# Performance work log

Hardware: AMD Instinct MI355X
Metric: run time of the kernel (lower is better)

The kernel has to match this reference:

```python
import jax, jax.numpy as jnp
import numpy as np
import math

B, N, D_IN, D_OUT, H = 8, 1024, 512, 512, 8
DH = D_OUT // H  # 64
SCALE = math.sqrt(DH)

def setup_inputs() -> dict:
    key = jax.random.key(0)
    ks = jax.random.split(key, 10)
    s_in = 1.0 / math.sqrt(D_IN)
    s_out = 1.0 / math.sqrt(D_OUT)
    return {
        "x": jax.random.normal(ks[0], (B, N, D_IN), dtype=jnp.float32),
        "Wq": jax.random.uniform(ks[1], (D_IN, D_OUT), jnp.float32, -s_in, s_in),
        "bq": jnp.zeros((D_OUT,), jnp.float32),
        "Wk": jax.random.uniform(ks[2], (D_IN, D_OUT), jnp.float32, -s_in, s_in),
        "bk": jnp.zeros((D_OUT,), jnp.float32),
        "Wv": jax.random.uniform(ks[3], (D_IN, D_OUT), jnp.float32, -s_in, s_in),
        "bv": jnp.zeros((D_OUT,), jnp.float32),
        "Wo": jax.random.uniform(ks[4], (D_OUT, D_OUT), jnp.float32, -s_out, s_out),
        "bo": jnp.zeros((D_OUT,), jnp.float32),
        # external distance-based positional bias buffer (num_heads, N, N)
        "pos_bias": 0.01 * jax.random.normal(ks[5], (H, N, N), dtype=jnp.float32),
    }

def reference(x, Wq, bq, Wk, bk, Wv, bv, Wo, bo, pos_bias):
    Bx, Nx, _ = x.shape
    # QKV projections -> (B, H, N, DH)
    def split_heads(t):
        return t.reshape(Bx, Nx, H, DH).transpose(0, 2, 1, 3)
    q = split_heads(x @ Wq + bq)
    k = split_heads(x @ Wk + bk)
    v = split_heads(x @ Wv + bv)
    # scaled dot-product scores with additive positional bias
    scores = jnp.einsum('bhnd,bhmd->bhnm', q, k) / SCALE + pos_bias[None]
    attn = jax.nn.softmax(scores, axis=-1)  # dropout p=0 (eval)
    out = jnp.einsum('bhnm,bhmd->bhnd', attn, v)
    out = out.transpose(0, 2, 1, 3).reshape(Bx, Nx, D_OUT)  # concat heads
    return out @ Wo + bo
```

## Files before the change

kernel.cpp:

```cpp
#include <hip/hip_runtime.h>
#include <hip/hip_bf16.h>
#include <hip/hip_fp8.h>
#include <stdint.h>


typedef __attribute__((ext_vector_type(4))) float f32x4;
typedef __attribute__((ext_vector_type(8))) short s16x8;
typedef __attribute__((ext_vector_type(4))) unsigned short u16x4;
typedef __attribute__((ext_vector_type(8))) unsigned short u16x8;

union FragAB { s16x8 v; u16x4 h[2]; unsigned u[4]; };

#define LOG2E 1.44269504089f
#define QSCALE (0.125f * LOG2E)
#define B8SCALE (64.0f * LOG2E)
#define B8INV 0.015625f

__device__ __forceinline__ unsigned short f2b(float f) {
  unsigned u = __builtin_bit_cast(unsigned, f);
  u = (u + 0x7FFFu + ((u >> 16) & 1u)) >> 16;
  return (unsigned short)u;
}
__device__ __forceinline__ unsigned cvt_pk(float a, float b) {
  unsigned r;
  asm("v_cvt_pk_bf16_f32 %0, %1, %2" : "=v"(r) : "v"(a), "v"(b));
  return r;
}
__device__ __forceinline__ float f8tof(unsigned b) {
  __hip_fp8_e4m3 v;
  v.__x = (__hip_fp8_storage_t)b;
  return (float)v;
}
__device__ __forceinline__ void gl_lds16(const unsigned short* g, unsigned short* l) {
  __builtin_amdgcn_global_load_lds(
      (const __attribute__((address_space(1))) unsigned int*)(g),
      (__attribute__((address_space(3))) unsigned int*)(l), 16, 0, 0);
}

__global__ __launch_bounds__(256) void prep_k(const float* __restrict__ x,
                                              unsigned short* __restrict__ xb,
                                              const float* __restrict__ W0,
                                              const float* __restrict__ W1,
                                              const float* __restrict__ W2,
                                              const float* __restrict__ W3,
                                              unsigned short* __restrict__ Wt,
                                              const float* __restrict__ pbias,
                                              unsigned char* __restrict__ pb8) {
  __shared__ float ld[64][68];
  const int t = threadIdx.x;
  if (blockIdx.x < 4096) {
    int idx = blockIdx.x * 256 + t;
    f32x4 v = ((const f32x4*)x)[idx];
    u16x4 o;
#pragma unroll
    for (int j = 0; j < 4; j++) o[j] = f2b(v[j]);
    ((u16x4*)xb)[idx] = o;
    return;
  }
  if (blockIdx.x >= 4352) {
    const int base = (blockIdx.x - 4352) * 4096 + t * 4;
#pragma unroll
    for (int u = 0; u < 4; u++) {
      const int idx = base + u * 1024;
      f32x4 v = *(const f32x4*)(pbias + idx);
      unsigned wds = 0;
#pragma unroll
      for (int j = 0; j < 4; j++) {
        __hip_fp8_e4m3 f(v[j] * B8SCALE);
        wds |= (unsigned)f.__x << (8 * j);
      }
      *(unsigned*)(pb8 + idx) = wds;
    }
    return;
  }
  const int bid2 = blockIdx.x - 4096;
  const int widx = bid2 >> 6;
  const int tile = bid2 & 63;
  const int trow = tile >> 3, tcol = tile & 7;
  const float* W = widx == 0 ? W0 : widx == 1 ? W1 : widx == 2 ? W2 : W3;
  const int r = t >> 2, cc = (t & 3) * 16;
  const float* src = W + (size_t)(trow * 64 + r) * 512 + tcol * 64 + cc;
#pragma unroll
  for (int u = 0; u < 4; u++)
    ((f32x4*)&ld[r][cc])[u] = ((const f32x4*)src)[u];
  __syncthreads();
  unsigned short* dst = Wt + ((size_t)widx << 18) + (size_t)(tcol * 64 + r) * 512 +
                        trow * 64 + cc;
#pragma unroll
  for (int u = 0; u < 4; u++) {
    u16x4 o;
#pragma unroll
    for (int e = 0; e < 4; e++) o[e] = f2b(ld[cc + u * 4 + e][r]);
    ((u16x4*)dst)[u] = o;
  }
}

__global__ __launch_bounds__(256, 2) void gemm_qkv_k(const unsigned short* __restrict__ A,
                                                     const unsigned short* __restrict__ Bt,
                                                     const float* __restrict__ bq,
                                                     const float* __restrict__ bk,
                                                     const float* __restrict__ bv,
                                                     unsigned short* __restrict__ outp) {
  __shared__ unsigned short SM[2][2][128][32];
  const int tid = threadIdx.x;
  const int lane = tid & 63;
  const int w = tid >> 6;
  const int wm = w >> 1, wn = w & 1;
  const int g = lane >> 4, c = lane & 15;
  const int bn0 = (blockIdx.x % 12) * 128;
  const int bm0 = (blockIdx.x / 12) * 128;

  f32x4 acc[4][4];
#pragma unroll
  for (int i = 0; i < 4; i++)
#pragma unroll
    for (int j = 0; j < 4; j++) acc[i][j] = f32x4{0.f, 0.f, 0.f, 0.f};

  auto stage = [&](int buf, int kt) {
#pragma unroll
    for (int j = 0; j < 2; j++) {
      const int qb = (j * 4 + w) * 64;
      const int chunk = qb + lane;
      const int row = chunk >> 2, slot = chunk & 3;
      gl_lds16(A + (size_t)(bm0 + row) * 512 + kt * 32 + slot * 8,
               &SM[buf][0][0][0] + qb * 8);
      gl_lds16(Bt + (size_t)(bn0 + row) * 512 + kt * 32 + slot * 8,
               &SM[buf][1][0][0] + qb * 8);
    }
  };

  stage(0, 0);
  asm volatile("s_waitcnt vmcnt(0)" ::: "memory");
  __syncthreads();

  for (int kt = 0; kt < 16; ++kt) {
    const int cb = kt & 1;
    if (kt < 15) stage(cb ^ 1, kt + 1);

    FragAB af[4], bf[4];
#pragma unroll
    for (int mi = 0; mi < 4; mi++) {
      const u16x4* p = (const u16x4*)&SM[cb][0][wm * 64 + mi * 16 + c][g * 8];
      af[mi].h[0] = p[0]; af[mi].h[1] = p[1];
    }
#pragma unroll
    for (int ni = 0; ni < 4; ni++) {
      const u16x4* p = (const u16x4*)&SM[cb][1][wn * 64 + ni * 16 + c][g * 8];
      bf[ni].h[0] = p[0]; bf[ni].h[1] = p[1];
    }
    __builtin_amdgcn_s_setprio(1);
#pragma unroll
    for (int mi = 0; mi < 4; mi++)
#pragma unroll
      for (int ni = 0; ni < 4; ni++)
        acc[mi][ni] = __builtin_amdgcn_mfma_f32_16x16x32_bf16(af[mi].v, bf[ni].v,
                                                              acc[mi][ni], 0, 0, 0);
    __builtin_amdgcn_s_setprio(0);

    if (kt < 15) {
      asm volatile("s_waitcnt vmcnt(0)" ::: "memory");
      __syncthreads();
    }
  }

  __syncthreads();

  const int qkv = (bn0 + wn * 64) >> 9;
  const float* bp = qkv == 0 ? bq : (qkv == 1 ? bk : bv);
  const float scale = qkv == 0 ? QSCALE : 1.0f;
  const int b = (bm0 + wm * 64) >> 10;
  const int nb = (bm0 + wm * 64) & 1023;

  if (qkv == 2) {
    unsigned short* T = &SM[0][0][0][0] + w * 2176;
    const int hh = ((bn0 + wn * 64) & 511) >> 6;
    unsigned short* dst = outp + ((size_t)2 << 22) + ((size_t)((b << 3) + hh) << 16) + nb;
#pragma unroll
    for (int r2 = 0; r2 < 2; r2++) {
#pragma unroll
      for (int ni2 = 0; ni2 < 2; ni2++) {
        const int ni = r2 * 2 + ni2;
        const int dloc = ni2 * 16 + c;
        const float bvv = bp[(bn0 + wn * 64 + ni * 16 + c) & 511];
#pragma unroll
        for (int mi = 0; mi < 4; mi++) {
          const int n = mi * 16 + g * 4;
          *(unsigned*)&T[dloc * 68 + n] =
              cvt_pk(acc[mi][ni][0] + bvv, acc[mi][ni][1] + bvv);
          *(unsigned*)&T[dloc * 68 + n + 2] =
              cvt_pk(acc[mi][ni][2] + bvv, acc[mi][ni][3] + bvv);
        }
      }
      asm volatile("s_waitcnt lgkmcnt(0)" ::: "memory");
#pragma unroll
      for (int r = 0; r < 8; r++) {
        const int dloc = r * 4 + g;
        const u16x4 v4 = *(const u16x4*)&T[dloc * 68 + c * 4];
        *(u16x4*)(dst + ((size_t)(r2 * 32 + dloc) << 10) + c * 4) = v4;
      }
      if (r2 == 0) asm volatile("s_waitcnt lgkmcnt(0)" ::: "memory");
    }
  } else {
#pragma unroll
    for (int mi = 0; mi < 4; mi++)
#pragma unroll
      for (int ni = 0; ni < 4; ni++) {
        const int c9 = (bn0 + wn * 64 + ni * 16 + c) & 511;
        const float bvv = bp[c9];
        const int hh = c9 >> 6, d = c9 & 63;
#pragma unroll
        for (int m = 0; m < 4; m++) {
          const int n = nb + mi * 16 + g * 4 + m;
          const float v = (acc[mi][ni][m] + bvv) * scale;
          outp[((size_t)qkv << 22) + ((size_t)((b << 3) + hh) << 16) +
               ((size_t)n << 6) + d] = f2b(v);
        }
      }
  }
}

__global__ __launch_bounds__(512, 2) void gemm_o_k(const unsigned short* __restrict__ A,
                                                   const unsigned short* __restrict__ Bt,
                                                   const float* __restrict__ bias,
                                                   float* __restrict__ outp) {
  __shared__ unsigned short SM[2][2][128][32];
  const int tid = threadIdx.x;
  const int lane = tid & 63;
  const int w = tid >> 6;
  const int wm = w >> 1, wn = w & 1;
  const int g = lane >> 4, c = lane & 15;
  const int bn0 = (blockIdx.x & 3) * 128;
  const int bm0 = (blockIdx.x >> 2) * 128;

  f32x4 acc[2][4];
#pragma unroll
  for (int i = 0; i < 2; i++)
#pragma unroll
    for (int j = 0; j < 4; j++) acc[i][j] = f32x4{0.f, 0.f, 0.f, 0.f};

  auto stage = [&](int buf, int kt) {
    const int qb = w * 64;
    const int chunk = qb + lane;
    const int row = chunk >> 2, slot = chunk & 3;
    gl_lds16(A + (size_t)(bm0 + row) * 512 + kt * 32 + slot * 8,
             &SM[buf][0][0][0] + qb * 8);
    gl_lds16(Bt + (size_t)(bn0 + row) * 512 + kt * 32 + slot * 8,
             &SM[buf][1][0][0] + qb * 8);
  };

  stage(0, 0);
  asm volatile("s_waitcnt vmcnt(0)" ::: "memory");
  __syncthreads();

  for (int kt = 0; kt < 16; ++kt) {
    const int cb = kt & 1;
    if (kt < 15) stage(cb ^ 1, kt + 1);

    FragAB af[2], bf[4];
#pragma unroll
    for (int mi = 0; mi < 2; mi++) {
      const u16x4* p = (const u16x4*)&SM[cb][0][wm * 32 + mi * 16 + c][g * 8];
      af[mi].h[0] = p[0]; af[mi].h[1] = p[1];
    }
#pragma unroll
    for (int ni = 0; ni < 4; ni++) {
      const u16x4* p = (const u16x4*)&SM[cb][1][wn * 64 + ni * 16 + c][g * 8];
      bf[ni].h[0] = p[0]; bf[ni].h[1] = p[1];
    }
    __builtin_amdgcn_s_setprio(1);
#pragma unroll
    for (int mi = 0; mi < 2; mi++)
#pragma unroll
      for (int ni = 0; ni < 4; ni++)
        acc[mi][ni] = __builtin_amdgcn_mfma_f32_16x16x32_bf16(af[mi].v, bf[ni].v,
                                                              acc[mi][ni], 0, 0, 0);
    __builtin_amdgcn_s_setprio(0);

    if (kt < 15) {
      asm volatile("s_waitcnt vmcnt(0)" ::: "memory");
      __syncthreads();
    }
  }

#pragma unroll
  for (int mi = 0; mi < 2; mi++) {
#pragma unroll
    for (int ni = 0; ni < 4; ni++) {
      const int col = bn0 + wn * 64 + ni * 16 + c;
      const float bv = bias[col];
#pragma unroll
      for (int m = 0; m < 4; m++) {
        const int row = bm0 + wm * 32 + mi * 16 + g * 4 + m;
        outp[(size_t)row * 512 + col] = acc[mi][ni][m] + bv;
      }
    }
  }
}

__global__ __launch_bounds__(256, 2) void attn_k(const unsigned short* __restrict__ Qb,
                                                 const unsigned short* __restrict__ Kb,
                                                 const unsigned short* __restrict__ Vt,
                                                 const unsigned char* __restrict__ pb8,
                                                 unsigned short* __restrict__ ao) {
  __shared__ unsigned short Klds[2][64][68];
  __shared__ unsigned short Vtlds[2][64][68];
  __shared__ unsigned short Plds[4][32][68];

  const int tid = threadIdx.x;
  const int lane = tid & 63;
  const int w = tid >> 6;
  const int g = lane >> 4, c = lane & 15;
  const int L = blockIdx.x;
  const int qt = L >> 6;
  const int bh = (L & 7) + 8 * ((L >> 3) & 7);
  const int h = bh & 7;
  const size_t bhq = (size_t)bh << 16;
  const int q0 = qt * 128 + w * 32;

  FragAB aq[2][2];
#pragma unroll
  for (int mi = 0; mi < 2; mi++)
#pragma unroll
    for (int kk = 0; kk < 2; kk++) {
      const u16x4* p = (const u16x4*)(Qb + bhq + ((size_t)(q0 + mi * 16 + c) << 6) +
                                      kk * 32 + g * 8);
      aq[mi][kk].h[0] = p[0]; aq[mi][kk].h[1] = p[1];
    }

  f32x4 acco[2][4];
#pragma unroll
  for (int mi = 0; mi < 2; mi++)
#pragma unroll
    for (int nd = 0; nd < 4; nd++) acco[mi][nd] = f32x4{0.f, 0.f, 0.f, 0.f};
  float lsum[2] = {0.f, 0.f};

  const int srow = tid >> 2;
  const int scol = (tid & 3) * 16;
  const unsigned short* pK = Kb + bhq + ((size_t)srow << 6) + scol;
  const unsigned short* pV = Vt + bhq + ((size_t)srow << 10) + scol;

  u16x8 kr0, kr1, vr0, vr1;
  auto stageLoad = [&](int k0n) {
    const u16x8* a = (const u16x8*)(pK + ((size_t)k0n << 6));
    kr0 = a[0]; kr1 = a[1];
    const u16x8* bb = (const u16x8*)(pV + k0n);
    vr0 = bb[0]; vr1 = bb[1];
  };
  auto stageWrite = [&](int b) {
    *(u16x8*)&Klds[b][srow][scol] = kr0;
    *(u16x8*)&Klds[b][srow][scol + 8] = kr1;
    *(u16x8*)&Vtlds[b][srow][scol] = vr0;
    *(u16x8*)&Vtlds[b][srow][scol + 8] = vr1;
  };

  const unsigned char* pbB = pb8 + ((size_t)h << 20) + ((size_t)(q0 + c) << 10) + 4 * g;

  stageLoad(0);
  stageWrite(0);
  __syncthreads();

  for (int kt = 0; kt < 16; ++kt) {
    const int buf = kt & 1;
    const int k0 = kt << 6;
    if (kt < 15) stageLoad(k0 + 64);

    unsigned pbw[2][4];
#pragma unroll
    for (int mi = 0; mi < 2; mi++)
#pragma unroll
      for (int ni = 0; ni < 4; ni++)
        pbw[mi][ni] = *(const unsigned*)(pbB + (mi << 14) + k0 + 16 * ni);

    FragAB bk[4][2];
#pragma unroll
    for (int ni = 0; ni < 4; ni++)
#pragma unroll
      for (int kk = 0; kk < 2; kk++) {
        const u16x4* p = (const u16x4*)&Klds[buf][ni * 16 + c][kk * 32 + g * 8];
        bk[ni][kk].h[0] = p[0]; bk[ni][kk].h[1] = p[1];
      }
    f32x4 sT[2][4];
    __builtin_amdgcn_s_setprio(1);
#pragma unroll
    for (int mi = 0; mi < 2; mi++)
#pragma unroll
      for (int ni = 0; ni < 4; ni++) {
        f32x4 s = f32x4{0.f, 0.f, 0.f, 0.f};
        s = __builtin_amdgcn_mfma_f32_16x16x32_bf16(bk[ni][0].v, aq[mi][0].v, s, 0, 0, 0);
        s = __builtin_amdgcn_mfma_f32_16x16x32_bf16(bk[ni][1].v, aq[mi][1].v, s, 0, 0, 0);
        sT[mi][ni] = s;
      }
    __builtin_amdgcn_s_setprio(0);

    FragAB vb2[4][2];
#pragma unroll
    for (int nd = 0; nd < 4; nd++)
#pragma unroll
      for (int kc = 0; kc < 2; kc++) {
        const u16x4* p = (const u16x4*)&Vtlds[buf][nd * 16 + c][kc * 32 + g * 8];
        vb2[nd][kc].h[0] = p[0]; vb2[nd][kc].h[1] = p[1];
      }

#pragma unroll
    for (int mi = 0; mi < 2; mi++)
#pragma unroll
      for (int ni = 0; ni < 4; ni++) {
        const unsigned wd = pbw[mi][ni];
        const float p0 =
            __builtin_amdgcn_exp2f(fmaf(f8tof(wd & 255u), B8INV, sT[mi][ni][0]));
        const float p1 =
            __builtin_amdgcn_exp2f(fmaf(f8tof((wd >> 8) & 255u), B8INV, sT[mi][ni][1]));
        const float p2 =
            __builtin_amdgcn_exp2f(fmaf(f8tof((wd >> 16) & 255u), B8INV, sT[mi][ni][2]));
        const float p3 =
            __builtin_amdgcn_exp2f(fmaf(f8tof(wd >> 24), B8INV, sT[mi][ni][3]));
        lsum[mi] += (p0 + p1) + (p2 + p3);
        uint2 two;
        two.x = cvt_pk(p0, p1);
        two.y = cvt_pk(p2, p3);
        *(uint2*)&Plds[w][mi * 16 + c][16 * ni + 4 * g] = two;
      }

    asm volatile("s_waitcnt lgkmcnt(0)" ::: "memory");

    FragAB paf[2][2];
#pragma unroll
    for (int mi = 0; mi < 2; mi++)
#pragma unroll
      for (int kc = 0; kc < 2; kc++) {
        const u16x4* p = (const u16x4*)&Plds[w][mi * 16 + c][kc * 32 + g * 8];
        paf[mi][kc].h[0] = p[0]; paf[mi][kc].h[1] = p[1];
      }
    __builtin_amdgcn_s_setprio(1);
#pragma unroll
    for (int mi = 0; mi < 2; mi++)
#pragma unroll
      for (int nd = 0; nd < 4; nd++) {
        acco[mi][nd] = __builtin_amdgcn_mfma_f32_16x16x32_bf16(paf[mi][0].v, vb2[nd][0].v,
                                                               acco[mi][nd], 0, 0, 0);
        acco[mi][nd] = __builtin_amdgcn_mfma_f32_16x16x32_bf16(paf[mi][1].v, vb2[nd][1].v,
                                                               acco[mi][nd], 0, 0, 0);
      }
    __builtin_amdgcn_s_setprio(0);

    if (kt < 15) {
      stageWrite(buf ^ 1);
      __syncthreads();
    }
  }

  const int b = bh >> 3;
#pragma unroll
  for (int mi = 0; mi < 2; mi++) {
    float l = lsum[mi];
    l += __shfl_xor(l, 16);
    l += __shfl_xor(l, 32);
    const float inv_c = 1.f / l;
#pragma unroll
    for (int m = 0; m < 4; m++) {
      const float invm = __shfl(inv_c, g * 4 + m);
      const int n = q0 + mi * 16 + g * 4 + m;
#pragma unroll
      for (int nd = 0; nd < 4; nd++) {
        ao[((size_t)(b * 1024 + n) << 9) + h * 64 + nd * 16 + c] =
            f2b(acco[mi][nd][m] * invm);
      }
    }
  }
}

extern "C" void kernel_launch(void* const* d_in, const int* in_sizes, int n_in,
                              void* d_out, int out_size, void* d_ws, size_t ws_size,
                              hipStream_t stream) {
  (void)in_sizes; (void)n_in; (void)out_size; (void)ws_size;
  const float* x  = (const float*)d_in[0];
  const float* Wq = (const float*)d_in[1];
  const float* bq = (const float*)d_in[2];
  const float* Wk = (const float*)d_in[3];
  const float* bk = (const float*)d_in[4];
  const float* Wv = (const float*)d_in[5];
  const float* bv = (const float*)d_in[6];
  const float* Wo = (const float*)d_in[7];
  const float* bo = (const float*)d_in[8];
  const float* pbias = (const float*)d_in[9];

  char* p = (char*)d_ws;
  unsigned short* xb  = (unsigned short*)p; p += (size_t)8192 * 512 * 2;
  unsigned short* WT  = (unsigned short*)p; p += (size_t)4 * 512 * 512 * 2;
  unsigned short* Qb  = (unsigned short*)p; p += (size_t)3 * 64 * 1024 * 64 * 2;
  unsigned short* AO  = (unsigned short*)p; p += (size_t)8192 * 512 * 2;
  unsigned char*  PB8 = (unsigned char*)p;

  unsigned short* WoT = WT + (size_t)3 * 512 * 512;
  unsigned short* Kb  = Qb + (size_t)64 * 1024 * 64;
  unsigned short* Vb  = Kb + (size_t)64 * 1024 * 64;

  prep_k<<<6400, 256, 0, stream>>>(x, xb, Wq, Wk, Wv, Wo, WT, pbias, PB8);
  gemm_qkv_k<<<768, 256, 0, stream>>>(xb, WT, bq, bk, bv, Qb);
  attn_k<<<512, 256, 0, stream>>>(Qb, Kb, Vb, PB8, AO);
  gemm_o_k<<<256, 512, 0, stream>>>(AO, WoT, bo, (float*)d_out);
}
```

Baseline: 85.64 us.

## Move pos-bias fp8 encode into QKV GEMM launch and use packed fp8 converts

```diff
diff --git a/kernel.cpp b/kernel.cpp
--- a/kernel.cpp
+++ b/kernel.cpp
@@ -1,9 +1,9 @@
 #include <hip/hip_runtime.h>
 #include <hip/hip_bf16.h>
-#include <hip/hip_fp8.h>
 #include <stdint.h>
 
 
+typedef __attribute__((ext_vector_type(2))) float f32x2;
 typedef __attribute__((ext_vector_type(4))) float f32x4;
 typedef __attribute__((ext_vector_type(8))) short s16x8;
 typedef __attribute__((ext_vector_type(4))) unsigned short u16x4;
@@ -26,10 +26,15 @@
   asm("v_cvt_pk_bf16_f32 %0, %1, %2" : "=v"(r) : "v"(a), "v"(b));
   return r;
 }
-__device__ __forceinline__ float f8tof(unsigned b) {
-  __hip_fp8_e4m3 v;
-  v.__x = (__hip_fp8_storage_t)b;
-  return (float)v;
+__device__ __forceinline__ f32x2 cvt2_f8(unsigned w) {
+  f32x2 r;
+  asm("v_cvt_pk_f32_fp8 %0, %1" : "=v"(r) : "v"(w));
+  return r;
+}
+__device__ __forceinline__ unsigned enc2_f8(float a, float b) {
+  unsigned r;
+  asm("v_cvt_pk_fp8_f32 %0, %1, %2" : "=v"(r) : "v"(a), "v"(b));
+  return r & 0xffffu;
 }
 __device__ __forceinline__ void gl_lds16(const unsigned short* g, unsigned short* l) {
   __builtin_amdgcn_global_load_lds(
@@ -43,9 +48,7 @@
                                               const float* __restrict__ W1,
                                               const float* __restrict__ W2,
                                               const float* __restrict__ W3,
-                                              unsigned short* __restrict__ Wt,
-                                              const float* __restrict__ pbias,
-                                              unsigned char* __restrict__ pb8) {
+                                              unsigned short* __restrict__ Wt) {
   __shared__ float ld[64][68];
   const int t = threadIdx.x;
   if (blockIdx.x < 4096) {
@@ -55,22 +58,6 @@
 #pragma unroll
     for (int j = 0; j < 4; j++) o[j] = f2b(v[j]);
     ((u16x4*)xb)[idx] = o;
-    return;
-  }
-  if (blockIdx.x >= 4352) {
-    const int base = (blockIdx.x - 4352) * 4096 + t * 4;
-#pragma unroll
-    for (int u = 0; u < 4; u++) {
-      const int idx = base + u * 1024;
-      f32x4 v = *(const f32x4*)(pbias + idx);
-      unsigned wds = 0;
-#pragma unroll
-      for (int j = 0; j < 4; j++) {
-        __hip_fp8_e4m3 f(v[j] * B8SCALE);
-        wds |= (unsigned)f.__x << (8 * j);
-      }
-      *(unsigned*)(pb8 + idx) = wds;
-    }
     return;
   }
   const int bid2 = blockIdx.x - 4096;
@@ -100,9 +87,25 @@
                                                      const float* __restrict__ bq,
                                                      const float* __restrict__ bk,
                                                      const float* __restrict__ bv,
-                                                     unsigned short* __restrict__ outp) {
+                                                     unsigned short* __restrict__ outp,
+                                                     const float* __restrict__ pbias,
+                                                     unsigned char* __restrict__ pb8) {
   __shared__ unsigned short SM[2][2][128][32];
   const int tid = threadIdx.x;
+
+  if (blockIdx.x >= 768) {
+    const int base = (blockIdx.x - 768) * 4096 + tid * 4;
+#pragma unroll
+    for (int u = 0; u < 4; u++) {
+      const int idx = base + u * 1024;
+      f32x4 v = *(const f32x4*)(pbias + idx);
+      const unsigned lo = enc2_f8(v[0] * B8SCALE, v[1] * B8SCALE);
+      const unsigned hi = enc2_f8(v[2] * B8SCALE, v[3] * B8SCALE);
+      *(unsigned*)(pb8 + idx) = lo | (hi << 16);
+    }
+    return;
+  }
+
   const int lane = tid & 63;
   const int w = tid >> 6;
   const int wm = w >> 1, wn = w & 1;
@@ -406,14 +409,12 @@
 #pragma unroll
       for (int ni = 0; ni < 4; ni++) {
         const unsigned wd = pbw[mi][ni];
-        const float p0 =
-            __builtin_amdgcn_exp2f(fmaf(f8tof(wd & 255u), B8INV, sT[mi][ni][0]));
-        const float p1 =
-            __builtin_amdgcn_exp2f(fmaf(f8tof((wd >> 8) & 255u), B8INV, sT[mi][ni][1]));
-        const float p2 =
-            __builtin_amdgcn_exp2f(fmaf(f8tof((wd >> 16) & 255u), B8INV, sT[mi][ni][2]));
-        const float p3 =
-            __builtin_amdgcn_exp2f(fmaf(f8tof(wd >> 24), B8INV, sT[mi][ni][3]));
+        const f32x2 blo = cvt2_f8(wd);
+        const f32x2 bhi = cvt2_f8(wd >> 16);
+        const float p0 = __builtin_amdgcn_exp2f(fmaf(blo[0], B8INV, sT[mi][ni][0]));
+        const float p1 = __builtin_amdgcn_exp2f(fmaf(blo[1], B8INV, sT[mi][ni][1]));
+        const float p2 = __builtin_amdgcn_exp2f(fmaf(bhi[0], B8INV, sT[mi][ni][2]));
+        const float p3 = __builtin_amdgcn_exp2f(fmaf(bhi[1], B8INV, sT[mi][ni][3]));
         lsum[mi] += (p0 + p1) + (p2 + p3);
         uint2 two;
         two.x = cvt_pk(p0, p1);
@@ -495,8 +496,8 @@
   unsigned short* Kb  = Qb + (size_t)64 * 1024 * 64;
   unsigned short* Vb  = Kb + (size_t)64 * 1024 * 64;
 
-  prep_k<<<6400, 256, 0, stream>>>(x, xb, Wq, Wk, Wv, Wo, WT, pbias, PB8);
-  gemm_qkv_k<<<768, 256, 0, stream>>>(xb, WT, bq, bk, bv, Qb);
+  prep_k<<<4352, 256, 0, stream>>>(x, xb, Wq, Wk, Wv, Wo, WT);
+  gemm_qkv_k<<<2816, 256, 0, stream>>>(xb, WT, bq, bk, bv, Qb, pbias, PB8);
   attn_k<<<512, 256, 0, stream>>>(Qb, Kb, Vb, PB8, AO);
   gemm_o_k<<<256, 512, 0, stream>>>(AO, WoT, bo, (float*)d_out);
 }
```

New measurement: 84.89 us. About the same (-0.9%).
